# Performance work log

Measured on AMD Instinct MI355X. Metric: run time of the kernel, lower is better.

## Reference

```python
import jax, jax.numpy as jnp
import numpy as np
from jax import lax

EPS = 1e-5


def fps(xyz, npoint):
    # Farthest point sampling; xyz [B, N, 3] -> idx [B, npoint] (starts at point 0)
    B, N, _ = xyz.shape

    def body(carry, _):
        dist, far = carry
        c = jnp.take_along_axis(xyz, far[:, None, None], axis=1)  # [B,1,3]
        d = jnp.sum((xyz - c) ** 2, -1)                            # [B,N]
        dist = jnp.minimum(dist, d)
        nxt = jnp.argmax(dist, -1).astype(jnp.int32)
        return (dist, nxt), far

    init = (jnp.full((B, N), 1e10, xyz.dtype), jnp.zeros((B,), jnp.int32))
    _, idx = lax.scan(body, init, None, length=npoint)
    return idx.T  # [B, npoint]


def query_ball(radius, nsample, xyz, new_xyz):
    # xyz [B,N,3], new_xyz [B,S,3] -> idx [B,S,nsample]
    N = xyz.shape[1]
    sqr = jnp.sum((new_xyz[:, :, None, :] - xyz[:, None, :, :]) ** 2, -1)  # [B,S,N]
    idx = jnp.where(sqr > radius * radius, N, jnp.arange(N)[None, None, :])
    idx = jnp.sort(idx, axis=-1)[:, :, :nsample]
    # out-of-ball slots get replaced by the first in-ball index (torch repo behavior)
    return jnp.where(idx == N, idx[:, :, :1], idx)


def gather_pts(x, idx):
    # x [B,N,C], idx [B,...] -> [B,...,C]
    B = x.shape[0]
    b = jnp.arange(B).reshape((B,) + (1,) * (idx.ndim - 1))
    return x[b, idx]


def mlp_bn(x, layers):
    # x [B,S,K,C]; shared 1x1-conv MLP + training-mode BatchNorm + ReLU
    for w, g, b in layers:
        x = jnp.einsum('bskc,oc->bsko', x, w)
        mean = x.mean((0, 1, 2))
        var = x.var((0, 1, 2))  # biased, as torch BN uses for normalization
        x = jax.nn.relu((x - mean) * lax.rsqrt(var + EPS) * g + b)
    return x


def set_abstraction(xyz, points, npoint, radius, nsample, layers, group_all):
    B = xyz.shape[0]
    if group_all:
        new_xyz = jnp.zeros((B, 1, 3), xyz.dtype)
        new_points = xyz[:, None]  # [B,1,N,3] (raw xyz, no centering)
        if points is not None:
            new_points = jnp.concatenate([new_points, points[:, None]], -1)
    else:
        fidx = fps(xyz, npoint)
        new_xyz = gather_pts(xyz, fidx)                     # [B,S,3]
        idx = query_ball(radius, nsample, xyz, new_xyz)     # [B,S,K]
        grouped = gather_pts(xyz, idx) - new_xyz[:, :, None, :]
        if points is not None:
            new_points = jnp.concatenate([grouped, gather_pts(points, idx)], -1)
        else:
            new_points = grouped
    feat = mlp_bn(new_points, layers).max(2)  # max-pool over neighbors -> [B,S,C]
    return new_xyz, feat


def _forward(xyz_time, l1, l2, l3):
    B, T, N, _ = xyz_time.shape
    x = xyz_time.reshape(B * T, N, 4)
    xyz, t = x[..., :3], x[..., 3:]
    x1_xyz, x1 = set_abstraction(xyz, t, 512, 0.2, 32, l1, False)
    x2_xyz, x2 = set_abstraction(x1_xyz, x1, 128, 0.4, 64, l2, False)
    _, x3 = set_abstraction(x2_xyz, x2, None, None, None, l3, True)
    return x3.reshape(B, T, -1)


def setup_inputs() -> dict:
    key = jax.random.key(0)
    ks = jax.random.split(key, 16)
    inp = {"xyz_time": jax.random.uniform(ks[0], (2, 4, 4096, 4), jnp.float32)}
    specs = {1: [(64, 4), (64, 64), (128, 64)],
             2: [(128, 131), (128, 128), (256, 128)],
             3: [(256, 259), (512, 256), (1024, 512)]}
    i = 1
    for s, layers in specs.items():
        for j, (o, c) in enumerate(layers):
            inp[f"w{s}_{j}"] = jax.random.normal(jax.random.fold_in(ks[i], j), (o, c), jnp.float32) * 0.1
            inp[f"g{s}_{j}"] = jnp.ones((o,), jnp.float32)
            inp[f"b{s}_{j}"] = jnp.zeros((o,), jnp.float32)
        i += 1
    return inp


def reference(xyz_time, w1_0, g1_0, b1_0, w1_1, g1_1, b1_1, w1_2, g1_2, b1_2,
              w2_0, g2_0, b2_0, w2_1, g2_1, b2_1, w2_2, g2_2, b2_2,
              w3_0, g3_0, b3_0, w3_1, g3_1, b3_1, w3_2, g3_2, b3_2):
    l1 = [(w1_0, g1_0, b1_0), (w1_1, g1_1, b1_1), (w1_2, g1_2, b1_2)]
    l2 = [(w2_0, g2_0, b2_0), (w2_1, g2_1, b2_1), (w2_2, g2_2, b2_2)]
    l3 = [(w3_0, g3_0, b3_0), (w3_1, g3_1, b3_1), (w3_2, g3_2, b3_2)]
    return _forward(xyz_time, l1, l2, l3)
```

## Files before the change

### kernel.cpp

```cpp
#include <hip/hip_runtime.h>


typedef short s16x8 __attribute__((ext_vector_type(8)));
typedef float f32x4 __attribute__((ext_vector_type(4)));

__device__ __forceinline__ unsigned short f2bf_rne(float f) {
    unsigned u = __float_as_uint(f);
    u += 0x7FFFu + ((u >> 16) & 1u);
    return (unsigned short)(u >> 16);
}
__device__ __forceinline__ void f2bf_split(float v, unsigned short& hi,
                                           unsigned short& lo) {
    unsigned u = __float_as_uint(v);
    unsigned r = u + 0x7FFFu + ((u >> 16) & 1u);
    hi = (unsigned short)(r >> 16);
    float vh = __uint_as_float(r & 0xFFFF0000u);
    lo = f2bf_rne(v - vh);
}

__device__ __forceinline__ unsigned long long umax64(unsigned long long a,
                                                     unsigned long long b) {
    return a > b ? a : b;
}

__device__ __forceinline__ unsigned wred_umax63(unsigned v) {
    unsigned t;
    t = (unsigned)__builtin_amdgcn_update_dpp(0, (int)v, 0x111, 0xf, 0xf, true); if (t > v) v = t;
    t = (unsigned)__builtin_amdgcn_update_dpp(0, (int)v, 0x112, 0xf, 0xf, true); if (t > v) v = t;
    t = (unsigned)__builtin_amdgcn_update_dpp(0, (int)v, 0x114, 0xf, 0xf, true); if (t > v) v = t;
    t = (unsigned)__builtin_amdgcn_update_dpp(0, (int)v, 0x118, 0xf, 0xf, true); if (t > v) v = t;
    t = (unsigned)__builtin_amdgcn_update_dpp(0, (int)v, 0x142, 0xa, 0xf, true); if (t > v) v = t;
    t = (unsigned)__builtin_amdgcn_update_dpp(0, (int)v, 0x143, 0xc, 0xf, true); if (t > v) v = t;
    return v;
}

__device__ __forceinline__ void wave_argmax(unsigned dbits, unsigned nInv,
                                            unsigned& vmax, unsigned& iInv) {
    unsigned m = wred_umax63(dbits);
    vmax = (unsigned)__builtin_amdgcn_readlane((int)m, 63);
    unsigned cand = (dbits == vmax) ? nInv : 0u;
    unsigned im = wred_umax63(cand);
    iInv = (unsigned)__builtin_amdgcn_readlane((int)im, 63);
}

struct PWArgs {
    const float* w[9];
    unsigned off[9];
    int O[9], C[9], CP[9];
};
__device__ __forceinline__ void prep_w_dev(const PWArgs& a,
                                           unsigned short* __restrict__ wh,
                                           unsigned short* __restrict__ wl,
                                           int i) {
    int l = 0;
#pragma unroll
    for (int k = 1; k < 9; ++k) if (i >= (int)a.off[k]) l = k;
    int li = i - (int)a.off[l];
    int CP = a.CP[l];
    int o = li / CP;
    int c = li - o * CP;
    float v = (c < a.C[l]) ? a.w[l][(size_t)o * a.C[l] + c] : 0.f;
    unsigned short h, lo;
    f2bf_split(v, h, lo);
    wh[i] = h; wl[i] = lo;
}

template<int NT, int ITEMS, int STRIDE>
__global__ __launch_bounds__(NT) void fps_block(
    const float* __restrict__ pts, int npoint,
    int* __restrict__ outIdx, float* __restrict__ outXyz,
    int nFps, PWArgs pw, unsigned short* __restrict__ wh,
    unsigned short* __restrict__ wl, int wtotal)
{
    constexpr int N = NT * ITEMS;
    constexpr int NW = NT / 64;
    __shared__ float4 scoord[N];
    __shared__ unsigned long long wkey[2][NW];

    if (blockIdx.x >= nFps) {
        int i = (blockIdx.x - nFps) * NT + threadIdx.x;
        if (i < wtotal) prep_w_dev(pw, wh, wl, i);
        return;
    }

    const int b = blockIdx.x;
    const int tid = threadIdx.x;
    const int wid = tid >> 6;
    const int lane = tid & 63;
    const float* P = pts + (size_t)b * N * STRIDE;

    float px[ITEMS], py[ITEMS], pz[ITEMS], dloc[ITEMS];
#pragma unroll
    for (int w = 0; w < ITEMS; ++w) {
        int n = tid + w * NT;
        float x, y, z;
        if (STRIDE == 4) {
            float4 v = *(const float4*)(P + (size_t)n * 4);
            x = v.x; y = v.y; z = v.z;
        } else {
            x = P[(size_t)n * STRIDE + 0];
            y = P[(size_t)n * STRIDE + 1];
            z = P[(size_t)n * STRIDE + 2];
        }
        px[w] = x; py[w] = y; pz[w] = z;
        scoord[n] = make_float4(x, y, z, 0.f);
        dloc[w] = 1e10f;
    }
    __syncthreads();
    float4 c0 = scoord[0];
    float cx = c0.x, cy = c0.y, cz = c0.z;
    int far = 0;

    for (int i = 0; i < npoint; ++i) {
        if (tid == 0) {
            outIdx[(size_t)b * npoint + i] = far;
            outXyz[((size_t)b * npoint + i) * 3 + 0] = cx;
            outXyz[((size_t)b * npoint + i) * 3 + 1] = cy;
            outXyz[((size_t)b * npoint + i) * 3 + 2] = cz;
        }
        float bestV = -1.0f;
        int bestW = 0;
#pragma unroll
        for (int w = 0; w < ITEMS; ++w) {
            float dx = __fsub_rn(px[w], cx);
            float dy = __fsub_rn(py[w], cy);
            float dz = __fsub_rn(pz[w], cz);
            float d = __fadd_rn(__fadd_rn(__fmul_rn(dx, dx), __fmul_rn(dy, dy)),
                                __fmul_rn(dz, dz));
            float dd = fminf(dloc[w], d);
            dloc[w] = dd;
            if (dd > bestV) { bestV = dd; bestW = w; }
        }
        int bestN = tid + bestW * NT;
        unsigned vmax, iInv;
        wave_argmax(__float_as_uint(bestV), 0xFFFFFFFFu ^ (unsigned)bestN,
                    vmax, iInv);
        const int par = i & 1;
        if (lane == 0)
            wkey[par][wid] = ((unsigned long long)vmax << 32) | iInv;
        __syncthreads();
        unsigned long long kb = wkey[par][0];
#pragma unroll
        for (int w2 = 1; w2 < NW; ++w2) kb = umax64(kb, wkey[par][w2]);
        far = (int)(0xFFFFFFFFu ^ (unsigned)kb);
        float4 cc = scoord[far];
        cx = cc.x; cy = cc.y; cz = cc.z;
    }
}

__device__ void fps_wave_dev(const float* __restrict__ pts, int npoint,
                             int* __restrict__ outIdx, float* __restrict__ outXyz,
                             int b, float4* scoord)
{
    constexpr int ITEMS = 8;
    constexpr int STRIDE = 3;
    constexpr int N = 64 * ITEMS;
    const int tid = threadIdx.x;
    const float* P = pts + (size_t)b * N * STRIDE;

    float px[ITEMS], py[ITEMS], pz[ITEMS], dloc[ITEMS];
#pragma unroll
    for (int w = 0; w < ITEMS; ++w) {
        int n = tid + w * 64;
        float x = P[(size_t)n * STRIDE + 0];
        float y = P[(size_t)n * STRIDE + 1];
        float z = P[(size_t)n * STRIDE + 2];
        px[w] = x; py[w] = y; pz[w] = z;
        scoord[n] = make_float4(x, y, z, 0.f);
        dloc[w] = 1e10f;
    }
    __threadfence_block();
    float4 c0 = scoord[0];
    float cx = c0.x, cy = c0.y, cz = c0.z;
    int far = 0;

    for (int i = 0; i < npoint; ++i) {
        if (tid == 0) {
            outIdx[(size_t)b * npoint + i] = far;
            outXyz[((size_t)b * npoint + i) * 3 + 0] = cx;
            outXyz[((size_t)b * npoint + i) * 3 + 1] = cy;
            outXyz[((size_t)b * npoint + i) * 3 + 2] = cz;
        }
        float bestV = -1.0f;
        int bestW = 0;
#pragma unroll
        for (int w = 0; w < ITEMS; ++w) {
            float dx = __fsub_rn(px[w], cx);
            float dy = __fsub_rn(py[w], cy);
            float dz = __fsub_rn(pz[w], cz);
            float d = __fadd_rn(__fadd_rn(__fmul_rn(dx, dx), __fmul_rn(dy, dy)),
                                __fmul_rn(dz, dz));
            float dd = fminf(dloc[w], d);
            dloc[w] = dd;
            if (dd > bestV) { bestV = dd; bestW = w; }
        }
        int bestN = tid + bestW * 64;
        unsigned vmax, iInv;
        wave_argmax(__float_as_uint(bestV), 0xFFFFFFFFu ^ (unsigned)bestN,
                    vmax, iInv);
        far = (int)(0xFFFFFFFFu ^ iInv);
        float4 cc = scoord[far];
        cx = cc.x; cy = cc.y; cz = cc.z;
    }
}

__global__ __launch_bounds__(256) void qb_group1(
    const float* __restrict__ xyz ,
    const float* __restrict__ ctr ,
    float* __restrict__ out )
{
    int gw = (blockIdx.x * 256 + threadIdx.x) >> 6;
    int lane = threadIdx.x & 63;
    if (gw >= 4096) return;
    int b = gw >> 9;
    const float* P = xyz + (size_t)b * 4096 * 4;
    float cx = ctr[(size_t)gw * 3 + 0];
    float cy = ctr[(size_t)gw * 3 + 1];
    float cz = ctr[(size_t)gw * 3 + 2];
    float* out0 = out + (size_t)gw * 32 * 8;
    int cnt = 0;
    float f0x = 0.f, f0y = 0.f, f0z = 0.f, f0t = 0.f;
    bool haveFirst = false;
    for (int base = 0; base < 4096 && cnt < 32; base += 64) {
        int n = base + lane;
        float4 p = *(const float4*)(P + (size_t)n * 4);
        float ex = __fsub_rn(p.x, cx);
        float ey = __fsub_rn(p.y, cy);
        float ez = __fsub_rn(p.z, cz);
        float d = __fadd_rn(__fadd_rn(__fmul_rn(ex, ex), __fmul_rn(ey, ey)),
                            __fmul_rn(ez, ez));
        bool inb = !(d > 0.04f);
        unsigned long long mask = __ballot(inb);
        if (mask) {
            if (!haveFirst) {
                int fl = (int)__builtin_ctzll(mask);
                f0x = __shfl(ex, fl); f0y = __shfl(ey, fl);
                f0z = __shfl(ez, fl); f0t = __shfl(p.w, fl);
                haveFirst = true;
            }
            if (inb) {
                int pos = cnt + __builtin_popcountll(mask & ((1ull << lane) - 1ull));
                if (pos < 32) {
                    float* o = out0 + (size_t)pos * 8;
                    *(float4*)o = make_float4(ex, ey, ez, p.w);
                    *(float4*)(o + 4) = make_float4(0.f, 0.f, 0.f, 0.f);
                }
            }
            cnt += (int)__builtin_popcountll(mask);
        }
    }
    if (cnt > 32) cnt = 32;
    for (int p2 = cnt + lane; p2 < 32; p2 += 64) {
        float* o = out0 + (size_t)p2 * 8;
        *(float4*)o = make_float4(f0x, f0y, f0z, f0t);
        *(float4*)(o + 4) = make_float4(0.f, 0.f, 0.f, 0.f);
    }
}

__global__ __launch_bounds__(256) void query_ball_kernel(
    const float* __restrict__ xyz, int stride, int N,
    const float* __restrict__ centers, int nCenters, int S,
    float r2, int nsample, int* __restrict__ outIdx)
{
    int gw = (blockIdx.x * 256 + threadIdx.x) >> 6;
    int lane = threadIdx.x & 63;
    if (gw >= nCenters) return;
    int b = gw / S;
    const float* P = xyz + (size_t)b * N * stride;
    float cx = centers[(size_t)gw * 3 + 0];
    float cy = centers[(size_t)gw * 3 + 1];
    float cz = centers[(size_t)gw * 3 + 2];
    int* out = outIdx + (size_t)gw * nsample;
    int cnt = 0;
    int firstIdx = 0;
    bool haveFirst = false;
    for (int base = 0; base < N && cnt < nsample; base += 64) {
        int n = base + lane;
        bool inb = false;
        if (n < N) {
            float dx = __fsub_rn(cx, P[(size_t)n * stride + 0]);
            float dy = __fsub_rn(cy, P[(size_t)n * stride + 1]);
            float dz = __fsub_rn(cz, P[(size_t)n * stride + 2]);
            float d = __fadd_rn(__fadd_rn(__fmul_rn(dx, dx), __fmul_rn(dy, dy)),
                                __fmul_rn(dz, dz));
            inb = !(d > r2);
        }
        unsigned long long mask = __ballot(inb);
        if (mask) {
            if (!haveFirst) { firstIdx = base + __builtin_ctzll(mask); haveFirst = true; }
            if (inb) {
                int pos = cnt + __builtin_popcountll(mask & ((1ull << lane) - 1ull));
                if (pos < nsample) out[pos] = n;
            }
            cnt += (int)__builtin_popcountll(mask);
        }
    }
    if (cnt > nsample) cnt = nsample;
    for (int p = cnt + lane; p < nsample; p += 64) out[p] = firstIdx;
}

__global__ __launch_bounds__(256) void group2_kernel(
    const float* __restrict__ xyz, const float* __restrict__ feat,
    const int* __restrict__ qb, const float* __restrict__ ctr,
    float* __restrict__ out)
{
    int i = blockIdx.x * 256 + threadIdx.x;
    if (i >= 65536 * 136) return;
    int sk = i / 136;
    int c = i - sk * 136;
    int b = sk / (128 * 64);
    int bs = sk / 64;
    int idx = qb[sk];
    idx = (idx < 0) ? 0 : (idx > 511 ? 511 : idx);
    float v = 0.f;
    if (c < 3)        v = __fsub_rn(xyz[((size_t)b * 512 + idx) * 3 + c], ctr[(size_t)bs * 3 + c]);
    else if (c < 131) v = feat[((size_t)b * 512 + idx) * 128 + (c - 3)];
    out[i] = v;
}

__global__ __launch_bounds__(256) void group3_kernel(
    const float* __restrict__ ctr2, const float* __restrict__ feat2,
    float* __restrict__ out)
{
    int i = blockIdx.x * 256 + threadIdx.x;
    if (i >= 1024 * 264) return;
    int sk = i / 264;
    int c = i - sk * 264;
    float v = 0.f;
    if (c < 3)        v = ctr2[(size_t)sk * 3 + c];
    else if (c < 259) v = feat2[(size_t)sk * 256 + (c - 3)];
    out[i] = v;
}

__global__ __launch_bounds__(256) void gemm_fused(
    const float* __restrict__ X,
    const float* __restrict__ scale, const float* __restrict__ shift,
    int applyAct,
    const unsigned short* __restrict__ Bh, const unsigned short* __restrict__ Bl,
    float* __restrict__ Y, double* __restrict__ part,
    int M, int AC, int CPW, int O, int YBmain,
    const float* __restrict__ fpsPts, int fpsNpoint,
    int* __restrict__ fpsIdx, float* __restrict__ fpsXyz)
{
    constexpr int PITCH = 40;
    __shared__ __align__(16) unsigned short sAh[128 * PITCH];
    __shared__ __align__(16) unsigned short sAl[128 * PITCH];
    __shared__ __align__(16) unsigned short sBh[128 * PITCH];
    __shared__ __align__(16) unsigned short sBl[128 * PITCH];
    __shared__ float sred[2048];

    if ((int)blockIdx.x >= YBmain) {
        if (threadIdx.x < 64 && fpsPts != nullptr)
            fps_wave_dev(fpsPts, fpsNpoint, fpsIdx, fpsXyz,
                         (int)blockIdx.x - YBmain, (float4*)sAh);
        return;
    }

    const int tid = threadIdx.x;
    const int lane = tid & 63;
    const int wid = tid >> 6;
    const int col15 = lane & 15;
    const int quad = lane >> 4;
    const int wm = (wid >> 1) * 64;
    const int wo = (wid & 1) * 64;
    const int m0 = blockIdx.x * 128;
    const int o0 = blockIdx.y * 128;
    const int YB = YBmain;
    const int lr = tid >> 2;
    const int lc = (tid & 3) * 8;

    f32x4 acc[4][4];
#pragma unroll
    for (int mt = 0; mt < 4; ++mt)
#pragma unroll
        for (int ot = 0; ot < 4; ++ot)
            acc[mt][ot] = {0.f, 0.f, 0.f, 0.f};

    for (int k0 = 0; k0 < CPW; k0 += 32) {
#pragma unroll
        for (int it = 0; it < 2; ++it) {
            int r = lr + it * 64;
            int c = k0 + lc;
            unsigned short h[8], l[8];
            if (c + 8 <= AC) {
                const float* xr = X + (size_t)(m0 + r) * AC + c;
                float4 v0 = *(const float4*)xr;
                float4 v1 = *(const float4*)(xr + 4);
                float vv[8] = {v0.x, v0.y, v0.z, v0.w, v1.x, v1.y, v1.z, v1.w};
#pragma unroll
                for (int j = 0; j < 8; ++j) {
                    float v = vv[j];
                    if (applyAct) v = fmaxf(v * scale[c + j] + shift[c + j], 0.f);
                    f2bf_split(v, h[j], l[j]);
                }
            } else {
#pragma unroll
                for (int j = 0; j < 8; ++j) { h[j] = 0; l[j] = 0; }
            }
            *(ushort4*)&sAh[r * PITCH + lc] = make_ushort4(h[0], h[1], h[2], h[3]);
            *(ushort4*)&sAh[r * PITCH + lc + 4] = make_ushort4(h[4], h[5], h[6], h[7]);
            *(ushort4*)&sAl[r * PITCH + lc] = make_ushort4(l[0], l[1], l[2], l[3]);
            *(ushort4*)&sAl[r * PITCH + lc + 4] = make_ushort4(l[4], l[5], l[6], l[7]);
        }
#pragma unroll
        for (int it = 0; it < 2; ++it) {
            int r = lr + it * 64;
            int c = k0 + lc;
            int o = o0 + r;
            uint4 vh = {0, 0, 0, 0}, vl = {0, 0, 0, 0};
            if (o < O && c < CPW) {
                size_t goff = (size_t)o * CPW + c;
                vh = *(const uint4*)(Bh + goff);
                vl = *(const uint4*)(Bl + goff);
            }
            *(uint4*)&sBh[r * PITCH + lc] = vh;
            *(uint4*)&sBl[r * PITCH + lc] = vl;
        }
        __syncthreads();
        s16x8 ah[4], al[4], bh[4], bl[4];
#pragma unroll
        for (int mt = 0; mt < 4; ++mt) {
            int rowoff = (wm + mt * 16 + col15) * PITCH + quad * 8;
            ah[mt] = *(const s16x8*)&sAh[rowoff];
            al[mt] = *(const s16x8*)&sAl[rowoff];
        }
#pragma unroll
        for (int ot = 0; ot < 4; ++ot) {
            int rowoff = (wo + ot * 16 + col15) * PITCH + quad * 8;
            bh[ot] = *(const s16x8*)&sBh[rowoff];
            bl[ot] = *(const s16x8*)&sBl[rowoff];
        }
#pragma unroll
        for (int mt = 0; mt < 4; ++mt)
#pragma unroll
            for (int ot = 0; ot < 4; ++ot) {
                acc[mt][ot] = __builtin_amdgcn_mfma_f32_16x16x32_bf16(
                    ah[mt], bl[ot], acc[mt][ot], 0, 0, 0);
                acc[mt][ot] = __builtin_amdgcn_mfma_f32_16x16x32_bf16(
                    al[mt], bh[ot], acc[mt][ot], 0, 0, 0);
                acc[mt][ot] = __builtin_amdgcn_mfma_f32_16x16x32_bf16(
                    ah[mt], bh[ot], acc[mt][ot], 0, 0, 0);
            }
        __syncthreads();
    }
#pragma unroll
    for (int mt = 0; mt < 4; ++mt)
#pragma unroll
        for (int ot = 0; ot < 4; ++ot) {
            int og = o0 + wo + ot * 16 + col15;
            if (og < O) {
#pragma unroll
                for (int r = 0; r < 4; ++r) {
                    int mg = m0 + wm + mt * 16 + quad * 4 + r;
                    Y[(size_t)mg * O + og] = acc[mt][ot][r];
                }
            }
        }
#pragma unroll
    for (int ot = 0; ot < 4; ++ot) {
        float s = 0.f, s2 = 0.f;
#pragma unroll
        for (int mt = 0; mt < 4; ++mt)
#pragma unroll
            for (int r = 0; r < 4; ++r) {
                float v = acc[mt][ot][r];
                s += v;
                s2 += v * v;
            }
        int slot = ((wid * 4 + quad) * 16 + col15) * 4 + ot;
        sred[slot * 2] = s;
        sred[slot * 2 + 1] = s2;
    }
    __syncthreads();
    if (tid < 128) {
        int col = tid;
        int o = o0 + col;
        if (o < O) {
            int cb = col >> 6;
            int ot = (col & 63) >> 4;
            int c15 = col & 15;
            double S = 0.0, S2 = 0.0;
#pragma unroll
            for (int wp = 0; wp < 2; ++wp) {
                int wd = cb + wp * 2;
#pragma unroll
                for (int q = 0; q < 4; ++q) {
                    int slot = ((wd * 4 + q) * 16 + c15) * 4 + ot;
                    S += (double)sred[slot * 2];
                    S2 += (double)sred[slot * 2 + 1];
                }
            }
            part[(size_t)o * YB + blockIdx.x] = S;
            part[(size_t)O * YB + (size_t)o * YB + blockIdx.x] = S2;
        }
    }
}

__global__ __launch_bounds__(256) void finalize_bn(
    const double* __restrict__ part, const float* __restrict__ g,
    const float* __restrict__ bb, float* __restrict__ scale,
    float* __restrict__ shift, int O, int YB, double invM)
{
    int o = blockIdx.x;
    int tid = threadIdx.x;
    double s = 0.0, s2 = 0.0;
    for (int yb = tid; yb < YB; yb += 256) {
        s  += part[(size_t)o * YB + yb];
        s2 += part[(size_t)O * YB + (size_t)o * YB + yb];
    }
    __shared__ double sd[512];
    sd[tid] = s;
    sd[256 + tid] = s2;
    __syncthreads();
#pragma unroll
    for (int st = 128; st > 0; st >>= 1) {
        if (tid < st) {
            sd[tid] += sd[tid + st];
            sd[256 + tid] += sd[256 + tid + st];
        }
        __syncthreads();
    }
    if (tid == 0) {
        double mean = sd[0] * invM;
        double var = sd[256] * invM - mean * mean;
        float varf = (float)var;
        if (varf < 0.f) varf = 0.f;
        float sc = g[o] * rsqrtf(varf + 1e-5f);
        scale[o] = sc;
        shift[o] = bb[o] - (float)mean * sc;
    }
}

__global__ __launch_bounds__(256) void bn_relu_max(
    const float* __restrict__ Y, const float* __restrict__ scale,
    const float* __restrict__ shift, float* __restrict__ out,
    int Stot, int K, int O)
{
    int idx = blockIdx.x * 256 + threadIdx.x;
    if (idx >= Stot * O) return;
    int s = idx / O;
    int o = idx - s * O;
    const float* base = Y + (size_t)s * K * O + o;
    float sc = scale[o], sh = shift[o];
    float mx = 0.f;
    for (int k = 0; k < K; ++k) {
        float v = base[(size_t)k * O] * sc + sh;
        v = fmaxf(v, 0.f);
        mx = fmaxf(mx, v);
    }
    out[idx] = mx;
}

extern "C" void kernel_launch(void* const* d_in, const int* in_sizes, int n_in,
                              void* d_out, int out_size, void* d_ws, size_t ws_size,
                              hipStream_t stream)
{
    const float* xin = (const float*)d_in[0];
    const float* w[9]; const float* g[9]; const float* bb[9];
    for (int i = 0; i < 9; ++i) {
        w[i]  = (const float*)d_in[1 + 3 * i];
        g[i]  = (const float*)d_in[2 + 3 * i];
        bb[i] = (const float*)d_in[3 + 3 * i];
    }

    char* base = (char*)d_ws;
    size_t off = 0;
    auto alloc = [&](size_t bytes) -> void* {
        void* p = base + off;
        off = (off + bytes + 255) & ~(size_t)255;
        return p;
    };
    const int OC[9][3] = {{64,4,8},{64,64,64},{128,64,64},
                          {128,131,136},{128,128,128},{256,128,128},
                          {256,259,264},{512,256,256},{1024,512,512}};
    size_t woff[10]; woff[0] = 0;
    for (int i = 0; i < 9; ++i) woff[i + 1] = woff[i] + (size_t)OC[i][0] * OC[i][2];

    int*    fps1   = (int*)alloc((size_t)4096 * 4);
    int*    fps2   = (int*)alloc((size_t)1024 * 4);
    int*    qb2    = (int*)alloc((size_t)65536 * 4);
    float*  nx1    = (float*)alloc((size_t)12288 * 4);
    float*  nx2    = (float*)alloc((size_t)3072 * 4);
    float*  feat1  = (float*)alloc((size_t)524288 * 4);
    float*  feat2  = (float*)alloc((size_t)262144 * 4);
    double* part   = (double*)alloc((size_t)262144 * 8);
    float*  scales = (float*)alloc((size_t)9 * 1024 * 4);
    float*  shifts = (float*)alloc((size_t)9 * 1024 * 4);
    unsigned short* WH = (unsigned short*)alloc(woff[9] * 2);
    unsigned short* WL = (unsigned short*)alloc(woff[9] * 2);
    const size_t zeroBytes = off;
    float*  XG = (float*)alloc((size_t)65536 * 136 * 4);
    float*  A  = (float*)alloc((size_t)16777216 * 4);
    if (off > ws_size) return;

    hipMemsetAsync(d_ws, 0, zeroBytes, stream);

    PWArgs pwa;
    for (int i = 0; i < 9; ++i) {
        pwa.w[i] = w[i]; pwa.off[i] = (unsigned)woff[i];
        pwa.O[i] = OC[i][0]; pwa.C[i] = OC[i][1]; pwa.CP[i] = OC[i][2];
    }
    const int nPrep = (int)((woff[9] + 255) / 256);

    fps_block<256, 16, 4><<<8 + nPrep, 256, 0, stream>>>(
        xin, 512, fps1, nx1, 8, pwa, WH, WL, (int)woff[9]);
    qb_group1<<<(4096 * 64) / 256, 256, 0, stream>>>(xin, nx1, XG);

    gemm_fused<<<dim3(1024, 1), 256, 0, stream>>>(XG, nullptr, nullptr, 0, WH + woff[0], WL + woff[0], A, part, 131072, 8, 8, 64, 1024, nullptr, 0, nullptr, nullptr);
    finalize_bn<<<64, 256, 0, stream>>>(part, g[0], bb[0], scales + 0 * 1024, shifts + 0 * 1024, 64, 1024, 1.0 / 131072.0);
    gemm_fused<<<dim3(1024, 1), 256, 0, stream>>>(A, scales + 0 * 1024, shifts + 0 * 1024, 1, WH + woff[1], WL + woff[1], XG, part, 131072, 64, 64, 64, 1024, nullptr, 0, nullptr, nullptr);
    finalize_bn<<<64, 256, 0, stream>>>(part, g[1], bb[1], scales + 1 * 1024, shifts + 1 * 1024, 64, 1024, 1.0 / 131072.0);
    gemm_fused<<<dim3(1024 + 8, 1), 256, 0, stream>>>(XG, scales + 1 * 1024, shifts + 1 * 1024, 1, WH + woff[2], WL + woff[2], A, part, 131072, 64, 64, 128, 1024, nx1, 128, fps2, nx2);
    finalize_bn<<<128, 256, 0, stream>>>(part, g[2], bb[2], scales + 2 * 1024, shifts + 2 * 1024, 128, 1024, 1.0 / 131072.0);
    bn_relu_max<<<(4096 * 128) / 256, 256, 0, stream>>>(A, scales + 2 * 1024, shifts + 2 * 1024, feat1, 4096, 32, 128);

    query_ball_kernel<<<(8 * 128 * 64) / 256, 256, 0, stream>>>(
        nx1, 3, 512, nx2, 8 * 128, 128, 0.16f, 64, qb2);
    group2_kernel<<<(65536 * 136) / 256, 256, 0, stream>>>(nx1, feat1, qb2, nx2, XG);

    gemm_fused<<<dim3(512, 1), 256, 0, stream>>>(XG, nullptr, nullptr, 0, WH + woff[3], WL + woff[3], A, part, 65536, 136, 136, 128, 512, nullptr, 0, nullptr, nullptr);
    finalize_bn<<<128, 256, 0, stream>>>(part, g[3], bb[3], scales + 3 * 1024, shifts + 3 * 1024, 128, 512, 1.0 / 65536.0);
    gemm_fused<<<dim3(512, 1), 256, 0, stream>>>(A, scales + 3 * 1024, shifts + 3 * 1024, 1, WH + woff[4], WL + woff[4], XG, part, 65536, 128, 128, 128, 512, nullptr, 0, nullptr, nullptr);
    finalize_bn<<<128, 256, 0, stream>>>(part, g[4], bb[4], scales + 4 * 1024, shifts + 4 * 1024, 128, 512, 1.0 / 65536.0);
    gemm_fused<<<dim3(512, 2), 256, 0, stream>>>(XG, scales + 4 * 1024, shifts + 4 * 1024, 1, WH + woff[5], WL + woff[5], A, part, 65536, 128, 128, 256, 512, nullptr, 0, nullptr, nullptr);
    finalize_bn<<<256, 256, 0, stream>>>(part, g[5], bb[5], scales + 5 * 1024, shifts + 5 * 1024, 256, 512, 1.0 / 65536.0);
    bn_relu_max<<<(1024 * 256) / 256, 256, 0, stream>>>(A, scales + 5 * 1024, shifts + 5 * 1024, feat2, 1024, 64, 256);

    group3_kernel<<<(1024 * 264) / 256, 256, 0, stream>>>(nx2, feat2, XG);

    gemm_fused<<<dim3(8, 2), 256, 0, stream>>>(XG, nullptr, nullptr, 0, WH + woff[6], WL + woff[6], A, part, 1024, 264, 264, 256, 8, nullptr, 0, nullptr, nullptr);
    finalize_bn<<<256, 256, 0, stream>>>(part, g[6], bb[6], scales + 6 * 1024, shifts + 6 * 1024, 256, 8, 1.0 / 1024.0);
    gemm_fused<<<dim3(8, 4), 256, 0, stream>>>(A, scales + 6 * 1024, shifts + 6 * 1024, 1, WH + woff[7], WL + woff[7], XG, part, 1024, 256, 256, 512, 8, nullptr, 0, nullptr, nullptr);
    finalize_bn<<<512, 256, 0, stream>>>(part, g[7], bb[7], scales + 7 * 1024, shifts + 7 * 1024, 512, 8, 1.0 / 1024.0);
    gemm_fused<<<dim3(8, 8), 256, 0, stream>>>(XG, scales + 7 * 1024, shifts + 7 * 1024, 1, WH + woff[8], WL + woff[8], A, part, 1024, 512, 512, 1024, 8, nullptr, 0, nullptr, nullptr);
    finalize_bn<<<1024, 256, 0, stream>>>(part, g[8], bb[8], scales + 8 * 1024, shifts + 8 * 1024, 1024, 8, 1.0 / 1024.0);
    bn_relu_max<<<(8 * 1024) / 256, 256, 0, stream>>>(A, scales + 8 * 1024, shifts + 8 * 1024, (float*)d_out, 8, 128, 1024);
}
```

Before: 826.1 us.

## Fold BN finalize into GEMM tail and co-schedule FPS and ball query in other kernels

Removes the separate finalize_bn launches. The last GEMM block, found with an atomic counter and threadfence, now reduces the partial sums and writes the BN scale and shift. The second-level FPS moves from the third GEMM into extra blocks of qb_group1, and query_ball moves into extra blocks of the first bn_relu_max. Together this cuts about ten kernel launches and their serialization gaps. The cost is a serial reduction in a single block at each GEMM's end and per-layer counters that must be zeroed before each run.

```diff
diff --git a/kernel.cpp b/kernel.cpp
--- a/kernel.cpp
+++ b/kernel.cpp
@@ -207,8 +207,17 @@
 __global__ __launch_bounds__(256) void qb_group1(
     const float* __restrict__ xyz ,
     const float* __restrict__ ctr ,
-    float* __restrict__ out )
-{
+    float* __restrict__ out ,
+    int nQb, const float* __restrict__ fpsPts,
+    int* __restrict__ fpsIdx, float* __restrict__ fpsXyz)
+{
+    __shared__ float4 scoord[512];
+    if ((int)blockIdx.x >= nQb) {
+        if (threadIdx.x < 64)
+            fps_wave_dev(fpsPts, 128, fpsIdx, fpsXyz,
+                         (int)blockIdx.x - nQb, scoord);
+        return;
+    }
     int gw = (blockIdx.x * 256 + threadIdx.x) >> 6;
     int lane = threadIdx.x & 63;
     if (gw >= 4096) return;
@@ -257,14 +266,12 @@
     }
 }
 
-__global__ __launch_bounds__(256) void query_ball_kernel(
-    const float* __restrict__ xyz, int stride, int N,
-    const float* __restrict__ centers, int nCenters, int S,
-    float r2, int nsample, int* __restrict__ outIdx)
-{
-    int gw = (blockIdx.x * 256 + threadIdx.x) >> 6;
-    int lane = threadIdx.x & 63;
-    if (gw >= nCenters) return;
+__device__ __forceinline__ void qb2_dev(
+    const float* __restrict__ xyz, const float* __restrict__ centers,
+    int* __restrict__ outIdx, int gw, int lane)
+{
+    const int N = 512, stride = 3, S = 128, nsample = 64;
+    const float r2 = 0.16f;
     int b = gw / S;
     const float* P = xyz + (size_t)b * N * stride;
     float cx = centers[(size_t)gw * 3 + 0];
@@ -338,9 +345,10 @@
     int applyAct,
     const unsigned short* __restrict__ Bh, const unsigned short* __restrict__ Bl,
     float* __restrict__ Y, double* __restrict__ part,
-    int M, int AC, int CPW, int O, int YBmain,
-    const float* __restrict__ fpsPts, int fpsNpoint,
-    int* __restrict__ fpsIdx, float* __restrict__ fpsXyz)
+    int AC, int CPW, int O,
+    const float* __restrict__ gvec, const float* __restrict__ bvec,
+    float* __restrict__ scOut, float* __restrict__ shOut,
+    double invM, unsigned* __restrict__ counter)
 {
     constexpr int PITCH = 40;
     __shared__ __align__(16) unsigned short sAh[128 * PITCH];
@@ -348,13 +356,7 @@
     __shared__ __align__(16) unsigned short sBh[128 * PITCH];
     __shared__ __align__(16) unsigned short sBl[128 * PITCH];
     __shared__ float sred[2048];
-
-    if ((int)blockIdx.x >= YBmain) {
-        if (threadIdx.x < 64 && fpsPts != nullptr)
-            fps_wave_dev(fpsPts, fpsNpoint, fpsIdx, fpsXyz,
-                         (int)blockIdx.x - YBmain, (float4*)sAh);
-        return;
-    }
+    __shared__ int sLast;
 
     const int tid = threadIdx.x;
     const int lane = tid & 63;
@@ -365,7 +367,7 @@
     const int wo = (wid & 1) * 64;
     const int m0 = blockIdx.x * 128;
     const int o0 = blockIdx.y * 128;
-    const int YB = YBmain;
+    const int YB = gridDim.x;
     const int lr = tid >> 2;
     const int lc = (tid & 3) * 8;
 
@@ -494,57 +496,60 @@
             part[(size_t)O * YB + (size_t)o * YB + blockIdx.x] = S2;
         }
     }
-}
-
-__global__ __launch_bounds__(256) void finalize_bn(
-    const double* __restrict__ part, const float* __restrict__ g,
-    const float* __restrict__ bb, float* __restrict__ scale,
-    float* __restrict__ shift, int O, int YB, double invM)
-{
-    int o = blockIdx.x;
-    int tid = threadIdx.x;
-    double s = 0.0, s2 = 0.0;
-    for (int yb = tid; yb < YB; yb += 256) {
-        s  += part[(size_t)o * YB + yb];
-        s2 += part[(size_t)O * YB + (size_t)o * YB + yb];
-    }
-    __shared__ double sd[512];
-    sd[tid] = s;
-    sd[256 + tid] = s2;
+
+    __threadfence();
+    if (tid == 0) {
+        unsigned prev = atomicAdd(counter, 1u);
+        sLast = (prev == gridDim.x * gridDim.y - 1u) ? 1 : 0;
+    }
     __syncthreads();
-#pragma unroll
-    for (int st = 128; st > 0; st >>= 1) {
-        if (tid < st) {
-            sd[tid] += sd[tid + st];
-            sd[256 + tid] += sd[256 + tid + st];
-        }
-        __syncthreads();
-    }
-    if (tid == 0) {
-        double mean = sd[0] * invM;
-        double var = sd[256] * invM - mean * mean;
-        float varf = (float)var;
-        if (varf < 0.f) varf = 0.f;
-        float sc = g[o] * rsqrtf(varf + 1e-5f);
-        scale[o] = sc;
-        shift[o] = bb[o] - (float)mean * sc;
+    if (sLast) {
+        for (int o = tid; o < O; o += 256) {
+            const double* ps = part + (size_t)o * YB;
+            const double* pq = part + (size_t)O * YB + (size_t)o * YB;
+            double s0 = 0.0, s1 = 0.0, s2a = 0.0, s3 = 0.0;
+            double q0 = 0.0, q1 = 0.0, q2 = 0.0, q3 = 0.0;
+            for (int yb = 0; yb < YB; yb += 4) {
+                s0 += ps[yb];     s1 += ps[yb + 1];
+                s2a += ps[yb + 2]; s3 += ps[yb + 3];
+                q0 += pq[yb];     q1 += pq[yb + 1];
+                q2 += pq[yb + 2]; q3 += pq[yb + 3];
+            }
+            double S = (s0 + s1) + (s2a + s3);
+            double S2 = (q0 + q1) + (q2 + q3);
+            double mean = S * invM;
+            double var = S2 * invM - mean * mean;
+            float varf = (float)var;
+            if (varf < 0.f) varf = 0.f;
+            float sc = gvec[o] * rsqrtf(varf + 1e-5f);
+            scOut[o] = sc;
+            shOut[o] = bvec[o] - (float)mean * sc;
+        }
     }
 }
 
 __global__ __launch_bounds__(256) void bn_relu_max(
     const float* __restrict__ Y, const float* __restrict__ scale,
     const float* __restrict__ shift, float* __restrict__ out,
-    int Stot, int K, int O)
-{
+    int Stot, int K, int O, int nMain,
+    const float* __restrict__ qbXyz, const float* __restrict__ qbCtr,
+    int* __restrict__ qbOut)
+{
+    if ((int)blockIdx.x >= nMain) {
+        int wid = threadIdx.x >> 6, lane = threadIdx.x & 63;
+        int gw = ((int)blockIdx.x - nMain) * 4 + wid;
+        if (gw < 1024) qb2_dev(qbXyz, qbCtr, qbOut, gw, lane);
+        return;
+    }
     int idx = blockIdx.x * 256 + threadIdx.x;
     if (idx >= Stot * O) return;
     int s = idx / O;
     int o = idx - s * O;
-    const float* base = Y + (size_t)s * K * O + o;
+    const float* basep = Y + (size_t)s * K * O + o;
     float sc = scale[o], sh = shift[o];
     float mx = 0.f;
     for (int k = 0; k < K; ++k) {
-        float v = base[(size_t)k * O] * sc + sh;
+        float v = basep[(size_t)k * O] * sc + sh;
         v = fmaxf(v, 0.f);
         mx = fmaxf(mx, v);
     }
@@ -586,6 +591,7 @@
     double* part   = (double*)alloc((size_t)262144 * 8);
     float*  scales = (float*)alloc((size_t)9 * 1024 * 4);
     float*  shifts = (float*)alloc((size_t)9 * 1024 * 4);
+    unsigned* ctrs = (unsigned*)alloc((size_t)16 * 4);
     unsigned short* WH = (unsigned short*)alloc(woff[9] * 2);
     unsigned short* WL = (unsigned short*)alloc(woff[9] * 2);
     const size_t zeroBytes = off;
@@ -602,37 +608,39 @@
     }
     const int nPrep = (int)((woff[9] + 255) / 256);
 
+    auto gemm = [&](const float* X, const float* sc, const float* sh, int act,
+                    int wi, float* Y, int YB, int OB, int AC, int CPW, int O,
+                    int li, double invM) {
+        gemm_fused<<<dim3(YB, OB), 256, 0, stream>>>(
+            X, sc, sh, act, WH + woff[wi], WL + woff[wi], Y, part,
+            AC, CPW, O, g[wi], bb[wi], scales + li * 1024, shifts + li * 1024,
+            invM, ctrs + li);
+    };
+
     fps_block<256, 16, 4><<<8 + nPrep, 256, 0, stream>>>(
         xin, 512, fps1, nx1, 8, pwa, WH, WL, (int)woff[9]);
-    qb_group1<<<(4096 * 64) / 256, 256, 0, stream>>>(xin, nx1, XG);
-
-    gemm_fused<<<dim3(1024, 1), 256, 0, stream>>>(XG, nullptr, nullptr, 0, WH + woff[0], WL + woff[0], A, part, 131072, 8, 8, 64, 1024, nullptr, 0, nullptr, nullptr);
-    finalize_bn<<<64, 256, 0, stream>>>(part, g[0], bb[0], scales + 0 * 1024, shifts + 0 * 1024, 64, 1024, 1.0 / 131072.0);
-    gemm_fused<<<dim3(1024, 1), 256, 0, stream>>>(A, scales + 0 * 1024, shifts + 0 * 1024, 1, WH + woff[1], WL + woff[1], XG, part, 131072, 64, 64, 64, 1024, nullptr, 0, nullptr, nullptr);
-    finalize_bn<<<64, 256, 0, stream>>>(part, g[1], bb[1], scales + 1 * 1024, shifts + 1 * 1024, 64, 1024, 1.0 / 131072.0);
-    gemm_fused<<<dim3(1024 + 8, 1), 256, 0, stream>>>(XG, scales + 1 * 1024, shifts + 1 * 1024, 1, WH + woff[2], WL + woff[2], A, part, 131072, 64, 64, 128, 1024, nx1, 128, fps2, nx2);
-    finalize_bn<<<128, 256, 0, stream>>>(part, g[2], bb[2], scales + 2 * 1024, shifts + 2 * 1024, 128, 1024, 1.0 / 131072.0);
-    bn_relu_max<<<(4096 * 128) / 256, 256, 0, stream>>>(A, scales + 2 * 1024, shifts + 2 * 1024, feat1, 4096, 32, 128);
-
-    query_ball_kernel<<<(8 * 128 * 64) / 256, 256, 0, stream>>>(
-        nx1, 3, 512, nx2, 8 * 128, 128, 0.16f, 64, qb2);
+    qb_group1<<<1024 + 8, 256, 0, stream>>>(xin, nx1, XG, 1024, nx1, fps2, nx2);
+
+    gemm(XG, nullptr, nullptr, 0, 0, A, 1024, 1, 8, 8, 64, 0, 1.0 / 131072.0);
+    gemm(A, scales + 0, shifts + 0, 1, 1, XG, 1024, 1, 64, 64, 64, 1, 1.0 / 131072.0);
+    gemm(XG, scales + 1024, shifts + 1024, 1, 2, A, 1024, 1, 64, 64, 128, 2, 1.0 / 131072.0);
+    bn_relu_max<<<2048 + 256, 256, 0, stream>>>(
+        A, scales + 2048, shifts + 2048, feat1, 4096, 32, 128, 2048,
+        nx1, nx2, qb2);
+
     group2_kernel<<<(65536 * 136) / 256, 256, 0, stream>>>(nx1, feat1, qb2, nx2, XG);
-
-    gemm_fused<<<dim3(512, 1), 256, 0, stream>>>(XG, nullptr, nullptr, 0, WH + woff[3], WL + woff[3], A, part, 65536, 136, 136, 128, 512, nullptr, 0, nullptr, nullptr);
-    finalize_bn<<<128, 256, 0, stream>>>(part, g[3], bb[3], scales + 3 * 1024, shifts + 3 * 1024, 128, 512, 1.0 / 65536.0);
-    gemm_fused<<<dim3(512, 1), 256, 0, stream>>>(A, scales + 3 * 1024, shifts + 3 * 1024, 1, WH + woff[4], WL + woff[4], XG, part, 65536, 128, 128, 128, 512, nullptr, 0, nullptr, nullptr);
-    finalize_bn<<<128, 256, 0, stream>>>(part, g[4], bb[4], scales + 4 * 1024, shifts + 4 * 1024, 128, 512, 1.0 / 65536.0);
-    gemm_fused<<<dim3(512, 2), 256, 0, stream>>>(XG, scales + 4 * 1024, shifts + 4 * 1024, 1, WH + woff[5], WL + woff[5], A, part, 65536, 128, 128, 256, 512, nullptr, 0, nullptr, nullptr);
-    finalize_bn<<<256, 256, 0, stream>>>(part, g[5], bb[5], scales + 5 * 1024, shifts + 5 * 1024, 256, 512, 1.0 / 65536.0);
-    bn_relu_max<<<(1024 * 256) / 256, 256, 0, stream>>>(A, scales + 5 * 1024, shifts + 5 * 1024, feat2, 1024, 64, 256);
-
-    group3_kernel<<<(1024 * 264) / 256, 256, 0, stream>>>(nx2, feat2, XG);
-
-    gemm_fused<<<dim3(8, 2), 256, 0, stream>>>(XG, nullptr, nullptr, 0, WH + woff[6], WL + woff[6], A, part, 1024, 264, 264, 256, 8, nullptr, 0, nullptr, nullptr);
-    finalize_bn<<<256, 256, 0, stream>>>(part, g[6], bb[6], scales + 6 * 1024, shifts + 6 * 1024, 256, 8, 1.0 / 1024.0);
-    gemm_fused<<<dim3(8, 4), 256, 0, stream>>>(A, scales + 6 * 1024, shifts + 6 * 1024, 1, WH + woff[7], WL + woff[7], XG, part, 1024, 256, 256, 512, 8, nullptr, 0, nullptr, nullptr);
-    finalize_bn<<<512, 256, 0, stream>>>(part, g[7], bb[7], scales + 7 * 1024, shifts + 7 * 1024, 512, 8, 1.0 / 1024.0);
-    gemm_fused<<<dim3(8, 8), 256, 0, stream>>>(XG, scales + 7 * 1024, shifts + 7 * 1024, 1, WH + woff[8], WL + woff[8], A, part, 1024, 512, 512, 1024, 8, nullptr, 0, nullptr, nullptr);
-    finalize_bn<<<1024, 256, 0, stream>>>(part, g[8], bb[8], scales + 8 * 1024, shifts + 8 * 1024, 1024, 8, 1.0 / 1024.0);
-    bn_relu_max<<<(8 * 1024) / 256, 256, 0, stream>>>(A, scales + 8 * 1024, shifts + 8 * 1024, (float*)d_out, 8, 128, 1024);
-}
+    gemm(XG, nullptr, nullptr, 0, 3, A, 512, 1, 136, 136, 128, 3, 1.0 / 65536.0);
+    gemm(A, scales + 3072, shifts + 3072, 1, 4, XG, 512, 1, 128, 128, 128, 4, 1.0 / 65536.0);
+    gemm(XG, scales + 4096, shifts + 4096, 1, 5, A, 512, 2, 128, 128, 256, 5, 1.0 / 65536.0);
+    bn_relu_max<<<(1024 * 256) / 256, 256, 0, stream>>>(
+        A, scales + 5120, shifts + 5120, feat2, 1024, 64, 256, 1024 * 256 / 256,
+        nullptr, nullptr, nullptr);
+
+    group3_kernel<<<(1024 * 264 + 255) / 256, 256, 0, stream>>>(nx2, feat2, XG);
+    gemm(XG, nullptr, nullptr, 0, 6, A, 8, 2, 264, 264, 256, 6, 1.0 / 1024.0);
+    gemm(A, scales + 6144, shifts + 6144, 1, 7, XG, 8, 4, 256, 256, 512, 7, 1.0 / 1024.0);
+    gemm(XG, scales + 7168, shifts + 7168, 1, 8, A, 8, 8, 512, 512, 1024, 8, 1.0 / 1024.0);
+    bn_relu_max<<<(8 * 1024) / 256, 256, 0, stream>>>(
+        A, scales + 8192, shifts + 8192, (float*)d_out, 8, 128, 1024,
+        (8 * 1024) / 256, nullptr, nullptr, nullptr);
+}
```

Result: slower. 1.817 ms (+120.0%).
